# Kernel tuning notes

Measured on AMD Instinct MI355X. Metric: run time of the kernel, lower is better.

## Reference

```python
import jax, jax.numpy as jnp
import numpy as np

N_HEADS = 16
EPS = 1e-6

def setup_inputs() -> dict:
    key = jax.random.key(0)
    k1, k2, k3 = jax.random.split(key, 3)
    B, T, D = 1, 2048, 1024
    x = jax.random.normal(k1, (B, T, D), dtype=jnp.float32)
    # torch nn.Linear weights have shape [out_features, in_features]
    w_qkv = jax.random.normal(k2, (3 * D, D), dtype=jnp.float32) * (1.0 / np.sqrt(D))
    w_out = jax.random.normal(k3, (D, D), dtype=jnp.float32) * (1.0 / np.sqrt(D))
    return {"x": x, "w_qkv": w_qkv, "w_out": w_out}

def reference(x, w_qkv, w_out):
    B, T, D = x.shape
    H = N_HEADS
    Hs = D // H
    qkv = x @ w_qkv.T                              # [B, T, 3D]
    # split_heads with Hs fixed -> 3*H head groups; chunk along head dim gives q,k,v
    qkv = qkv.reshape(B, T, 3, H, Hs).transpose(2, 0, 3, 1, 4)  # [3, B, H, T, Hs]
    q, k, v = qkv[0], qkv[1], qkv[2]
    phi = lambda t: jax.nn.elu(t) + 1.0
    q, k = phi(q), phi(k)
    # causal linear attention (mask=None path): cumulative kv outer products
    k_cumsum = jnp.cumsum(k, axis=2)                           # [B, H, T, Hs]
    kv = jnp.einsum('bhtd,bhtf->bhtdf', k, v)                  # [B, H, T, Hs, Hs]
    kv_cumsum = jnp.cumsum(kv, axis=2)
    q_kv = jnp.einsum('bhtd,bhtdf->bhtf', q, kv_cumsum)        # [B, H, T, Hs]
    q_k_sum = jnp.einsum('bhtd,bhtd->bht', q, k_cumsum)        # [B, H, T]
    xo = q_kv / (q_k_sum[..., None] + EPS)                     # [B, H, T, Hs]
    xo = xo.transpose(0, 2, 1, 3).reshape(B, T, D)             # cat_heads
    return xo @ w_out.T
```

## Files before the change

kernel.cpp:

```cpp
#include <hip/hip_runtime.h>
#include <cmath>

#define T_SEQ 2048
#define HEADS 16
#define HS 64
#define NC 32
#define K2 2048
#define D_MODEL 1024

typedef __attribute__((ext_vector_type(4))) float f32x4;
typedef __attribute__((ext_vector_type(8))) unsigned short u16x8;
typedef __attribute__((ext_vector_type(4))) unsigned short u16x4;

__device__ __forceinline__ unsigned short f2bf_rne(float f){
  unsigned u = __builtin_bit_cast(unsigned, f);
  return (unsigned short)((u + 0x7FFFu + ((u >> 16) & 1u)) >> 16);
}
__device__ __forceinline__ float bf2f(unsigned short h){
  unsigned u = ((unsigned)h) << 16;
  return __builtin_bit_cast(float, u);
}

__global__ __launch_bounds__(256)
void split_all(const float* __restrict__ x, const float* __restrict__ wqkv,
               const float* __restrict__ wout,
               unsigned short* __restrict__ X2, unsigned short* __restrict__ Wq2,
               unsigned short* __restrict__ Wo2)
{
  const int b = blockIdx.x;
  const float* src; unsigned short* dst; int q0;
  if (b < 2048)      { src = x;    dst = X2;  q0 = b; }
  else if (b < 5120) { src = wqkv; dst = Wq2; q0 = b - 2048; }
  else               { src = wout; dst = Wo2; q0 = b - 5120; }
  const int q = q0 * 256 + threadIdx.x;
  float4 v = ((const float4*)src)[q];
  float f[4] = {v.x, v.y, v.z, v.w};
  u16x4 hi, lo;
  #pragma unroll
  for (int i = 0; i < 4; ++i){
    unsigned short h = f2bf_rne(f[i]);
    hi[i] = h;
    lo[i] = f2bf_rne(f[i] - bf2f(h));
  }
  size_t row = (size_t)(q >> 8);
  int c4 = (q & 255) * 4;
  *(u16x4*)(dst + row * K2 + c4) = hi;
  *(u16x4*)(dst + row * K2 + D_MODEL + c4) = lo;
}

__device__ __forceinline__ void gload_lds16(const unsigned short* g, void* l){
  __builtin_amdgcn_global_load_lds((const __attribute__((address_space(1))) unsigned int*)g,
                                   (__attribute__((address_space(3))) unsigned int*)l,
                                   16, 0, 0);
}

__device__ __forceinline__ void mfma_bf16(f32x4& d, u16x8 a, u16x8 b){
  asm("v_mfma_f32_16x16x32_bf16 %0, %1, %2, %0" : "+v"(d) : "v"(a), "v"(b));
}

template<int BM, int EPI>
__global__ __launch_bounds__(256, (BM == 128) ? 2 : 3)
void gemm_split3(const unsigned short* __restrict__ A2,
                 const unsigned short* __restrict__ B2,
                 float* __restrict__ C, int N,
                 float* __restrict__ qkvws)
{
  constexpr int AT = BM * 128;
  constexpr int MI = BM / 32;
  __shared__ unsigned char lds[2 * AT + 32768];

  const int bid = blockIdx.x;
  int bx, by;
  if constexpr (EPI == 1) {
    int swz = (bid & 7) * 48 + (bid >> 3);
    bx = swz >> 4; by = swz & 15;
  } else {
    int swz = (bid & 7) * 32 + (bid >> 3);
    bx = swz >> 5; by = swz & 31;
  }
  const int tileM = by * BM;
  const int tileN = bx * 128;

  const int tid  = threadIdx.x;
  const int lane = tid & 63;
  const int wid  = tid >> 6;
  const int wr   = (wid >> 1) * (BM / 2);
  const int wc   = (wid & 1) * 64;

  f32x4 acc[MI][4];
  #pragma unroll
  for (int i = 0; i < MI; ++i)
    #pragma unroll
    for (int j = 0; j < 4; ++j) acc[i][j] = (f32x4)0.f;

  const int srow = tid >> 3;
  const int kbp  = (tid & 7) << 4;
  const int skb  = kbp ^ ((srow & 7) << 4);
  const unsigned short* Arow = A2 + (size_t)(tileM + srow) * K2 + (skb >> 1);
  const unsigned short* Brow = B2 + (size_t)(tileN + srow) * K2 + (skb >> 1);
  unsigned char* dA = lds + tid * 16;

  #pragma unroll 1
  for (int kt = 0; kt < 16; ++kt){
    const int a_k = kt << 6;
    __syncthreads();
    #pragma unroll
    for (int i = 0; i < MI; ++i){
      gload_lds16(Arow + a_k + (size_t)i * 32 * K2,           dA + i * 4096);
      gload_lds16(Arow + D_MODEL + a_k + (size_t)i * 32 * K2, dA + AT + i * 4096);
    }
    #pragma unroll
    for (int i = 0; i < 4; ++i){
      gload_lds16(Brow + a_k + (size_t)i * 32 * K2,           dA + 2 * AT + i * 4096);
      gload_lds16(Brow + D_MODEL + a_k + (size_t)i * 32 * K2, dA + 2 * AT + 16384 + i * 4096);
    }
    __syncthreads();

    #pragma unroll
    for (int ks = 0; ks < 2; ++ks){
      u16x8 ah[MI], al[MI], bh[4], bl[4];
      #pragma unroll
      for (int mi = 0; mi < MI; ++mi){
        int row = wr + mi * 16 + (lane & 15);
        int kb  = ((ks << 6) + ((lane >> 4) << 4)) ^ ((row & 7) << 4);
        ah[mi] = *(const u16x8*)(lds + row * 128 + kb);
        al[mi] = *(const u16x8*)(lds + AT + row * 128 + kb);
      }
      #pragma unroll
      for (int ni = 0; ni < 4; ++ni){
        int row = wc + ni * 16 + (lane & 15);
        int kb  = ((ks << 6) + ((lane >> 4) << 4)) ^ ((row & 7) << 4);
        bh[ni] = *(const u16x8*)(lds + 2 * AT + row * 128 + kb);
        bl[ni] = *(const u16x8*)(lds + 2 * AT + 16384 + row * 128 + kb);
      }
      #pragma unroll
      for (int mi = 0; mi < MI; ++mi)
        #pragma unroll
        for (int ni = 0; ni < 4; ++ni){
          mfma_bf16(acc[mi][ni], ah[mi], bh[ni]);
          mfma_bf16(acc[mi][ni], ah[mi], bl[ni]);
          mfma_bf16(acc[mi][ni], al[mi], bh[ni]);
        }
    }
  }

  const int r0 = (lane >> 4) << 2;
  const int cl = lane & 15;
  if constexpr (EPI == 0) {
    #pragma unroll
    for (int mi = 0; mi < MI; ++mi){
      int gr = tileM + wr + mi * 16 + r0;
      #pragma unroll
      for (int ni = 0; ni < 4; ++ni){
        int gc = tileN + wc + ni * 16 + cl;
        #pragma unroll
        for (int r = 0; r < 4; ++r) C[(size_t)(gr + r) * N + gc] = acc[mi][ni][r];
      }
    }
  } else {
    #pragma unroll
    for (int ni = 0; ni < 4; ++ni){
      int gc = tileN + wc + ni * 16 + cl;
      int c3 = gc >> 10;
      int hh = (gc >> 6) & 15;
      int s  = gc & 63;
      float* dst = qkvws + ((size_t)(c3 * HEADS + hh) * T_SEQ) * HS + s;
      #pragma unroll
      for (int mi = 0; mi < MI; ++mi){
        int gr = tileM + wr + mi * 16 + r0;
        #pragma unroll
        for (int r = 0; r < 4; ++r){
          float v = acc[mi][ni][r];
          if (c3 < 2) v = (v > 0.f) ? (v + 1.f) : expf(v);
          dst[(size_t)(gr + r) * HS] = v;
        }
      }
    }
  }
}

__global__ __launch_bounds__(256)
void chunk_kv(const float* __restrict__ kbuf, const float* __restrict__ vbuf,
              float* __restrict__ Sc, float* __restrict__ Zc)
{
  const int h = blockIdx.x, c = blockIdx.y;
  const int tid = threadIdx.x;
  const int f = tid & 63, dg = tid >> 6;
  const size_t base = ((size_t)h * T_SEQ + c * 64) * HS;
  float s[16] = {};
  float z = 0.f;
  for (int t = 0; t < 64; ++t) {
    const float vv = vbuf[base + t * HS + f];
    const float* krow = kbuf + base + t * HS + dg * 16;
    float kk4[16];
    #pragma unroll
    for (int r4 = 0; r4 < 4; ++r4)
      *(float4*)&kk4[r4 * 4] = *(const float4*)&krow[r4 * 4];
    #pragma unroll
    for (int r = 0; r < 16; ++r) s[r] += kk4[r] * vv;
    if (dg == 0) z += kbuf[base + t * HS + f];
  }
  float* Sp = Sc + ((size_t)h * NC + c) * (HS * HS);
  #pragma unroll
  for (int r = 0; r < 16; ++r) Sp[(dg * 16 + r) * HS + f] = s[r];
  if (dg == 0) Zc[((size_t)h * NC + c) * HS + f] = z;
}

__global__ __launch_bounds__(256)
void scan_chunks(float* __restrict__ Sc, float* __restrict__ Zc)
{
  const int h = blockIdx.x;
  const int e = blockIdx.y * 256 + threadIdx.x;
  float* p = Sc + ((size_t)h * NC) * (HS * HS) + e;
  float run = 0.f;
  for (int c = 0; c < NC; ++c) {
    float v = p[(size_t)c * HS * HS]; p[(size_t)c * HS * HS] = run; run += v;
  }
  if (blockIdx.y == 0 && threadIdx.x < HS) {
    float* z = Zc + (size_t)h * NC * HS + threadIdx.x;
    float run2 = 0.f;
    for (int c = 0; c < NC; ++c) { float v = z[c * HS]; z[c * HS] = run2; run2 += v; }
  }
}

__global__ __launch_bounds__(256)
void chunk_attn(const float* __restrict__ qbuf, const float* __restrict__ kbuf,
                const float* __restrict__ vbuf, const float* __restrict__ Sc,
                const float* __restrict__ Zc, unsigned short* __restrict__ XO2)
{
  __shared__ float kT[HS][64];
  __shared__ float vl[64][HS + 1];
  __shared__ float Al[64][64];
  const int h = blockIdx.x, c = blockIdx.y;
  const int tid = threadIdx.x;
  const size_t base = ((size_t)h * T_SEQ + c * 64) * HS;

  {
    const int t0 = tid >> 2;
    const int cq = (tid & 3) * 4;
    #pragma unroll
    for (int it = 0; it < 4; ++it) {
      const int col = cq + it * 16;
      float kv[4]; *(float4*)kv = *(const float4*)&kbuf[base + (size_t)t0 * HS + col];
      float vv[4]; *(float4*)vv = *(const float4*)&vbuf[base + (size_t)t0 * HS + col];
      #pragma unroll
      for (int u = 0; u < 4; ++u) { kT[col + u][t0] = kv[u]; vl[t0][col + u] = vv[u]; }
    }
  }
  __syncthreads();

  const int j  = tid & 63;
  const int ig = tid >> 6;

  for (int r = 0; r < 16; ++r) {
    const int i = r * 4 + ig;
    const float* qrow = qbuf + base + (size_t)i * HS;
    float s0 = 0.f, s1 = 0.f, s2 = 0.f, s3 = 0.f;
    #pragma unroll
    for (int d = 0; d < HS; d += 4) {
      float qv[4]; *(float4*)qv = *(const float4*)&qrow[d];
      s0 += qv[0] * kT[d + 0][j];
      s1 += qv[1] * kT[d + 1][j];
      s2 += qv[2] * kT[d + 2][j];
      s3 += qv[3] * kT[d + 3][j];
    }
    Al[i][j] = (j <= i) ? ((s0 + s1) + (s2 + s3)) : 0.f;
  }
  __syncthreads();

  const int f = j;
  const float* Sp = Sc + ((size_t)h * NC + c) * (HS * HS);
  const float* Zp = Zc + ((size_t)h * NC + c) * HS;
  float num[16], den[16];

  for (int r = 0; r < 16; ++r) {
    const int i = r * 4 + ig;
    const float* qrow = qbuf + base + (size_t)i * HS;
    float n0=0.f,n1=0.f,n2=0.f,n3=0.f, e0=0.f,e1=0.f,e2=0.f,e3=0.f;
    #pragma unroll
    for (int d = 0; d < HS; d += 4) {
      float qv[4]; *(float4*)qv = *(const float4*)&qrow[d];
      n0 += qv[0] * Sp[(d + 0) * HS + f];  e0 += qv[0] * Zp[d + 0];
      n1 += qv[1] * Sp[(d + 1) * HS + f];  e1 += qv[1] * Zp[d + 1];
      n2 += qv[2] * Sp[(d + 2) * HS + f];  e2 += qv[2] * Zp[d + 2];
      n3 += qv[3] * Sp[(d + 3) * HS + f];  e3 += qv[3] * Zp[d + 3];
    }
    num[r] = (n0 + n1) + (n2 + n3);
    den[r] = (e0 + e1) + (e2 + e3);
  }

  for (int jj4 = 0; jj4 < 16; ++jj4) {
    float vv[4];
    #pragma unroll
    for (int u = 0; u < 4; ++u) vv[u] = vl[jj4 * 4 + u][f];
    #pragma unroll
    for (int r = 0; r < 16; ++r) {
      const int i = r * 4 + ig;
      float a[4]; *(float4*)a = *(const float4*)&Al[i][jj4 * 4];
      #pragma unroll
      for (int u = 0; u < 4; ++u) { num[r] += a[u] * vv[u]; den[r] += a[u]; }
    }
  }

  #pragma unroll
  for (int r = 0; r < 16; ++r) {
    const int i = r * 4 + ig;
    float val = num[r] / (den[r] + 1e-6f);
    unsigned short hb = f2bf_rne(val);
    unsigned short lb = f2bf_rne(val - bf2f(hb));
    size_t rowoff = (size_t)(c * 64 + i) * K2 + h * 64 + f;
    XO2[rowoff] = hb;
    XO2[rowoff + D_MODEL] = lb;
  }
}

extern "C" void kernel_launch(void* const* d_in, const int* in_sizes, int n_in,
                              void* d_out, int out_size, void* d_ws, size_t ws_size,
                              hipStream_t stream)
{
  (void)in_sizes; (void)n_in; (void)out_size; (void)ws_size;
  const float* x     = (const float*)d_in[0];
  const float* w_qkv = (const float*)d_in[1];
  const float* w_out = (const float*)d_in[2];
  float* out = (float*)d_out;
  char* wsb = (char*)d_ws;

  float* qbuf = (float*)(wsb);
  float* kbuf = (float*)(wsb + ((size_t)8  << 20));
  float* vbuf = (float*)(wsb + ((size_t)16 << 20));
  unsigned short* X2  = (unsigned short*)(wsb + ((size_t)24 << 20));
  float*          Sc  = (float*)(wsb + ((size_t)24 << 20));
  unsigned short* Wq2 = (unsigned short*)(wsb + ((size_t)32 << 20));
  float*          Zc  = (float*)(wsb + ((size_t)32 << 20));
  unsigned short* XO2 = (unsigned short*)(wsb + ((size_t)33 << 20));
  unsigned short* Wo2 = (unsigned short*)(wsb + ((size_t)44 << 20));

  split_all<<<6144, 256, 0, stream>>>(x, w_qkv, w_out, X2, Wq2, Wo2);
  gemm_split3<128, 1><<<384, 256, 0, stream>>>(X2, Wq2, nullptr, 3072, qbuf);
  chunk_kv<<<dim3(16, 32), 256, 0, stream>>>(kbuf, vbuf, Sc, Zc);
  scan_chunks<<<dim3(16, 16), 256, 0, stream>>>(Sc, Zc);
  chunk_attn<<<dim3(16, 32), 256, 0, stream>>>(qbuf, kbuf, vbuf, Sc, Zc, XO2);
  gemm_split3<64, 0><<<256, 256, 0, stream>>>(XO2, Wo2, out, 1024, nullptr);
}
```

Baseline: 217.7 us.

## Move chunked linear-attention stages onto split-bf16 MFMA with transposed layouts

```diff
diff --git a/kernel.cpp b/kernel.cpp
--- a/kernel.cpp
+++ b/kernel.cpp
@@ -25,9 +25,23 @@
 void split_all(const float* __restrict__ x, const float* __restrict__ wqkv,
                const float* __restrict__ wout,
                unsigned short* __restrict__ X2, unsigned short* __restrict__ Wq2,
-               unsigned short* __restrict__ Wo2)
+               unsigned short* __restrict__ Wo2, unsigned short* __restrict__ VT2)
 {
   const int b = blockIdx.x;
+  if (b >= 6144) {
+    int g   = (b - 6144) * 2048 + threadIdx.x * 8;
+    int hh  = g >> 16;
+    int rem = g & 65535;
+    int fi  = rem >> 12;
+    int pl  = (rem >> 11) & 1;
+    int t   = rem & 2047;
+    u16x8 val;
+    unsigned short fill = (fi == 0 && pl == 0) ? (unsigned short)0x3F80 : (unsigned short)0;
+    #pragma unroll
+    for (int e = 0; e < 8; ++e) val[e] = fill;
+    *(u16x8*)(VT2 + ((size_t)((hh * 80 + 64 + fi) * 2 + pl)) * 2048 + t) = val;
+    return;
+  }
   const float* src; unsigned short* dst; int q0;
   if (b < 2048)      { src = x;    dst = X2;  q0 = b; }
   else if (b < 5120) { src = wqkv; dst = Wq2; q0 = b - 2048; }
@@ -63,7 +77,8 @@
 void gemm_split3(const unsigned short* __restrict__ A2,
                  const unsigned short* __restrict__ B2,
                  float* __restrict__ C, int N,
-                 float* __restrict__ qkvws)
+                 unsigned short* __restrict__ Q2, unsigned short* __restrict__ K2k,
+                 unsigned short* __restrict__ kT2, unsigned short* __restrict__ VT2)
 {
   constexpr int AT = BM * 128;
   constexpr int MI = BM / 32;
@@ -164,15 +179,31 @@
       int c3 = gc >> 10;
       int hh = (gc >> 6) & 15;
       int s  = gc & 63;
-      float* dst = qkvws + ((size_t)(c3 * HEADS + hh) * T_SEQ) * HS + s;
       #pragma unroll
       for (int mi = 0; mi < MI; ++mi){
-        int gr = tileM + wr + mi * 16 + r0;
+        int gr0 = tileM + wr + mi * 16 + r0;
+        u16x4 h4, l4;
         #pragma unroll
         for (int r = 0; r < 4; ++r){
           float v = acc[mi][ni][r];
           if (c3 < 2) v = (v > 0.f) ? (v + 1.f) : expf(v);
-          dst[(size_t)(gr + r) * HS] = v;
+          unsigned short hb = f2bf_rne(v);
+          h4[r] = hb;
+          l4[r] = f2bf_rne(v - bf2f(hb));
+        }
+        if (c3 == 0){
+          unsigned short* Qb = Q2 + ((size_t)hh * T_SEQ + gr0) * 128 + s;
+          #pragma unroll
+          for (int r = 0; r < 4; ++r){ Qb[(size_t)r * 128] = h4[r]; Qb[(size_t)r * 128 + 64] = l4[r]; }
+        } else if (c3 == 1){
+          unsigned short* Kb = K2k + ((size_t)hh * T_SEQ + gr0) * 128 + s;
+          #pragma unroll
+          for (int r = 0; r < 4; ++r){ Kb[(size_t)r * 128] = h4[r]; Kb[(size_t)r * 128 + 64] = l4[r]; }
+          *(u16x4*)(kT2 + ((size_t)((hh * 64 + s) * 2 + 0)) * T_SEQ + gr0) = h4;
+          *(u16x4*)(kT2 + ((size_t)((hh * 64 + s) * 2 + 1)) * T_SEQ + gr0) = l4;
+        } else {
+          *(u16x4*)(VT2 + ((size_t)((hh * 80 + s) * 2 + 0)) * T_SEQ + gr0) = h4;
+          *(u16x4*)(VT2 + ((size_t)((hh * 80 + s) * 2 + 1)) * T_SEQ + gr0) = l4;
         }
       }
     }
@@ -180,137 +211,178 @@
 }
 
 __global__ __launch_bounds__(256)
-void chunk_kv(const float* __restrict__ kbuf, const float* __restrict__ vbuf,
-              float* __restrict__ Sc, float* __restrict__ Zc)
-{
-  const int h = blockIdx.x, c = blockIdx.y;
-  const int tid = threadIdx.x;
-  const int f = tid & 63, dg = tid >> 6;
-  const size_t base = ((size_t)h * T_SEQ + c * 64) * HS;
-  float s[16] = {};
-  float z = 0.f;
-  for (int t = 0; t < 64; ++t) {
-    const float vv = vbuf[base + t * HS + f];
-    const float* krow = kbuf + base + t * HS + dg * 16;
-    float kk4[16];
-    #pragma unroll
-    for (int r4 = 0; r4 < 4; ++r4)
-      *(float4*)&kk4[r4 * 4] = *(const float4*)&krow[r4 * 4];
-    #pragma unroll
-    for (int r = 0; r < 16; ++r) s[r] += kk4[r] * vv;
-    if (dg == 0) z += kbuf[base + t * HS + f];
-  }
-  float* Sp = Sc + ((size_t)h * NC + c) * (HS * HS);
-  #pragma unroll
-  for (int r = 0; r < 16; ++r) Sp[(dg * 16 + r) * HS + f] = s[r];
-  if (dg == 0) Zc[((size_t)h * NC + c) * HS + f] = z;
+void chunk_kv_mfma(const unsigned short* __restrict__ VT2,
+                   const unsigned short* __restrict__ kT2,
+                   float* __restrict__ Sc)
+{
+  const int bid = blockIdx.x;
+  const int swz = (bid & 7) * 64 + (bid >> 3);
+  const int h = swz >> 5, c = swz & 31;
+  const int lane = threadIdx.x & 63, w = threadIdx.x >> 6;
+  const int li = lane & 15, hq = lane >> 4;
+  const int bt = c * 64;
+
+  f32x4 acc[5];
+  #pragma unroll
+  for (int mt = 0; mt < 5; ++mt) acc[mt] = (f32x4)0.f;
+
+  const unsigned short* Kb = kT2 + ((size_t)((h * 64 + 16 * w + li) * 2)) * T_SEQ + bt;
+  u16x8 bh[2], bl[2];
+  #pragma unroll
+  for (int ks = 0; ks < 2; ++ks){
+    bh[ks] = *(const u16x8*)(Kb + ks * 32 + hq * 8);
+    bl[ks] = *(const u16x8*)(Kb + T_SEQ + ks * 32 + hq * 8);
+  }
+  #pragma unroll
+  for (int mt = 0; mt < 5; ++mt){
+    const unsigned short* Ab = VT2 + ((size_t)((h * 80 + 16 * mt + li) * 2)) * T_SEQ + bt;
+    #pragma unroll
+    for (int ks = 0; ks < 2; ++ks){
+      u16x8 ah = *(const u16x8*)(Ab + ks * 32 + hq * 8);
+      u16x8 al = *(const u16x8*)(Ab + T_SEQ + ks * 32 + hq * 8);
+      mfma_bf16(acc[mt], ah, bh[ks]);
+      mfma_bf16(acc[mt], ah, bl[ks]);
+      mfma_bf16(acc[mt], al, bh[ks]);
+    }
+  }
+  float* Sp = Sc + ((size_t)(h * 32 + c) * 80) * 64;
+  #pragma unroll
+  for (int mt = 0; mt < 5; ++mt){
+    int f = 16 * mt + 4 * hq;
+    #pragma unroll
+    for (int r = 0; r < 4; ++r)
+      Sp[(size_t)(f + r) * 64 + 16 * w + li] = acc[mt][r];
+  }
 }
 
 __global__ __launch_bounds__(256)
-void scan_chunks(float* __restrict__ Sc, float* __restrict__ Zc)
+void scan_chunks2(const float* __restrict__ Sc, unsigned short* __restrict__ SpT2)
 {
   const int h = blockIdx.x;
   const int e = blockIdx.y * 256 + threadIdx.x;
-  float* p = Sc + ((size_t)h * NC) * (HS * HS) + e;
+  const int f = e >> 6, d = e & 63;
+  unsigned short* Op = SpT2 + ((size_t)(h * 32) * 80 + f) * 128 + d;
+  if (f > 64){
+    for (int c = 0; c < NC; ++c){ Op[0] = 0; Op[64] = 0; Op += (size_t)80 * 128; }
+    return;
+  }
+  const float* Ip = Sc + ((size_t)(h * 32) * 80 + f) * 64 + d;
   float run = 0.f;
-  for (int c = 0; c < NC; ++c) {
-    float v = p[(size_t)c * HS * HS]; p[(size_t)c * HS * HS] = run; run += v;
-  }
-  if (blockIdx.y == 0 && threadIdx.x < HS) {
-    float* z = Zc + (size_t)h * NC * HS + threadIdx.x;
-    float run2 = 0.f;
-    for (int c = 0; c < NC; ++c) { float v = z[c * HS]; z[c * HS] = run2; run2 += v; }
+  for (int c = 0; c < NC; ++c){
+    unsigned short hb = f2bf_rne(run);
+    Op[0]  = hb;
+    Op[64] = f2bf_rne(run - bf2f(hb));
+    run += Ip[0];
+    Ip += (size_t)80 * 64;
+    Op += (size_t)80 * 128;
   }
 }
 
 __global__ __launch_bounds__(256)
-void chunk_attn(const float* __restrict__ qbuf, const float* __restrict__ kbuf,
-                const float* __restrict__ vbuf, const float* __restrict__ Sc,
-                const float* __restrict__ Zc, unsigned short* __restrict__ XO2)
-{
-  __shared__ float kT[HS][64];
-  __shared__ float vl[64][HS + 1];
-  __shared__ float Al[64][64];
-  const int h = blockIdx.x, c = blockIdx.y;
-  const int tid = threadIdx.x;
-  const size_t base = ((size_t)h * T_SEQ + c * 64) * HS;
-
-  {
-    const int t0 = tid >> 2;
-    const int cq = (tid & 3) * 4;
-    #pragma unroll
-    for (int it = 0; it < 4; ++it) {
-      const int col = cq + it * 16;
-      float kv[4]; *(float4*)kv = *(const float4*)&kbuf[base + (size_t)t0 * HS + col];
-      float vv[4]; *(float4*)vv = *(const float4*)&vbuf[base + (size_t)t0 * HS + col];
-      #pragma unroll
-      for (int u = 0; u < 4; ++u) { kT[col + u][t0] = kv[u]; vl[t0][col + u] = vv[u]; }
-    }
-  }
+void chunk_attn_mfma(const unsigned short* __restrict__ Q2,
+                     const unsigned short* __restrict__ K2k,
+                     const unsigned short* __restrict__ VT2,
+                     const unsigned short* __restrict__ SpT2,
+                     unsigned short* __restrict__ XO2)
+{
+  __shared__ unsigned short Pl[64][136];
+  const int bid = blockIdx.x;
+  const int swz = (bid & 7) * 64 + (bid >> 3);
+  const int h = swz >> 5, c = swz & 31;
+  const int lane = threadIdx.x & 63, w = threadIdx.x >> 6;
+  const int li = lane & 15, hq = lane >> 4;
+  const int bt = c * 64;
+
+  const unsigned short* Qp = Q2 + ((size_t)h * T_SEQ + bt + 16 * w + li) * 128;
+  u16x8 qh[2], ql[2];
+  #pragma unroll
+  for (int ks = 0; ks < 2; ++ks){
+    qh[ks] = *(const u16x8*)(Qp + ks * 32 + hq * 8);
+    ql[ks] = *(const u16x8*)(Qp + 64 + ks * 32 + hq * 8);
+  }
+
+  f32x4 accs[4];
+  #pragma unroll
+  for (int nt = 0; nt < 4; ++nt) accs[nt] = (f32x4)0.f;
+  #pragma unroll
+  for (int nt = 0; nt < 4; ++nt){
+    const unsigned short* Kp = K2k + ((size_t)h * T_SEQ + bt + 16 * nt + li) * 128;
+    #pragma unroll
+    for (int ks = 0; ks < 2; ++ks){
+      u16x8 kh = *(const u16x8*)(Kp + ks * 32 + hq * 8);
+      u16x8 kl = *(const u16x8*)(Kp + 64 + ks * 32 + hq * 8);
+      mfma_bf16(accs[nt], qh[ks], kh);
+      mfma_bf16(accs[nt], qh[ks], kl);
+      mfma_bf16(accs[nt], ql[ks], kh);
+    }
+  }
+
+  #pragma unroll
+  for (int nt = 0; nt < 4; ++nt){
+    int i0 = 16 * w + 4 * hq;
+    int j  = 16 * nt + li;
+    #pragma unroll
+    for (int r = 0; r < 4; ++r){
+      float v = (j <= i0 + r) ? accs[nt][r] : 0.f;
+      unsigned short hb = f2bf_rne(v);
+      Pl[i0 + r][j]      = hb;
+      Pl[i0 + r][64 + j] = f2bf_rne(v - bf2f(hb));
+    }
+  }
+
+  f32x4 acco[5];
+  #pragma unroll
+  for (int nt = 0; nt < 5; ++nt) acco[nt] = (f32x4)0.f;
+  const unsigned short* Sb = SpT2 + ((size_t)(h * 32 + c) * 80) * 128;
+  #pragma unroll
+  for (int nt = 0; nt < 5; ++nt){
+    const unsigned short* Sp = Sb + (size_t)(16 * nt + li) * 128;
+    #pragma unroll
+    for (int ks = 0; ks < 2; ++ks){
+      u16x8 sh = *(const u16x8*)(Sp + ks * 32 + hq * 8);
+      u16x8 sl = *(const u16x8*)(Sp + 64 + ks * 32 + hq * 8);
+      mfma_bf16(acco[nt], qh[ks], sh);
+      mfma_bf16(acco[nt], qh[ks], sl);
+      mfma_bf16(acco[nt], ql[ks], sh);
+    }
+  }
+
   __syncthreads();
 
-  const int j  = tid & 63;
-  const int ig = tid >> 6;
-
-  for (int r = 0; r < 16; ++r) {
-    const int i = r * 4 + ig;
-    const float* qrow = qbuf + base + (size_t)i * HS;
-    float s0 = 0.f, s1 = 0.f, s2 = 0.f, s3 = 0.f;
-    #pragma unroll
-    for (int d = 0; d < HS; d += 4) {
-      float qv[4]; *(float4*)qv = *(const float4*)&qrow[d];
-      s0 += qv[0] * kT[d + 0][j];
-      s1 += qv[1] * kT[d + 1][j];
-      s2 += qv[2] * kT[d + 2][j];
-      s3 += qv[3] * kT[d + 3][j];
-    }
-    Al[i][j] = (j <= i) ? ((s0 + s1) + (s2 + s3)) : 0.f;
-  }
-  __syncthreads();
-
-  const int f = j;
-  const float* Sp = Sc + ((size_t)h * NC + c) * (HS * HS);
-  const float* Zp = Zc + ((size_t)h * NC + c) * HS;
-  float num[16], den[16];
-
-  for (int r = 0; r < 16; ++r) {
-    const int i = r * 4 + ig;
-    const float* qrow = qbuf + base + (size_t)i * HS;
-    float n0=0.f,n1=0.f,n2=0.f,n3=0.f, e0=0.f,e1=0.f,e2=0.f,e3=0.f;
-    #pragma unroll
-    for (int d = 0; d < HS; d += 4) {
-      float qv[4]; *(float4*)qv = *(const float4*)&qrow[d];
-      n0 += qv[0] * Sp[(d + 0) * HS + f];  e0 += qv[0] * Zp[d + 0];
-      n1 += qv[1] * Sp[(d + 1) * HS + f];  e1 += qv[1] * Zp[d + 1];
-      n2 += qv[2] * Sp[(d + 2) * HS + f];  e2 += qv[2] * Zp[d + 2];
-      n3 += qv[3] * Sp[(d + 3) * HS + f];  e3 += qv[3] * Zp[d + 3];
-    }
-    num[r] = (n0 + n1) + (n2 + n3);
-    den[r] = (e0 + e1) + (e2 + e3);
-  }
-
-  for (int jj4 = 0; jj4 < 16; ++jj4) {
-    float vv[4];
-    #pragma unroll
-    for (int u = 0; u < 4; ++u) vv[u] = vl[jj4 * 4 + u][f];
-    #pragma unroll
-    for (int r = 0; r < 16; ++r) {
-      const int i = r * 4 + ig;
-      float a[4]; *(float4*)a = *(const float4*)&Al[i][jj4 * 4];
-      #pragma unroll
-      for (int u = 0; u < 4; ++u) { num[r] += a[u] * vv[u]; den[r] += a[u]; }
-    }
-  }
-
-  #pragma unroll
-  for (int r = 0; r < 16; ++r) {
-    const int i = r * 4 + ig;
-    float val = num[r] / (den[r] + 1e-6f);
-    unsigned short hb = f2bf_rne(val);
-    unsigned short lb = f2bf_rne(val - bf2f(hb));
-    size_t rowoff = (size_t)(c * 64 + i) * K2 + h * 64 + f;
-    XO2[rowoff] = hb;
-    XO2[rowoff + D_MODEL] = lb;
+  u16x8 ph[2], plo[2];
+  #pragma unroll
+  for (int ks = 0; ks < 2; ++ks){
+    ph[ks]  = *(const u16x8*)&Pl[16 * w + li][ks * 32 + hq * 8];
+    plo[ks] = *(const u16x8*)&Pl[16 * w + li][64 + ks * 32 + hq * 8];
+  }
+  #pragma unroll
+  for (int nt = 0; nt < 5; ++nt){
+    const unsigned short* Vp = VT2 + ((size_t)((h * 80 + 16 * nt + li) * 2)) * T_SEQ + bt;
+    #pragma unroll
+    for (int ks = 0; ks < 2; ++ks){
+      u16x8 vh = *(const u16x8*)(Vp + ks * 32 + hq * 8);
+      u16x8 vl = *(const u16x8*)(Vp + T_SEQ + ks * 32 + hq * 8);
+      mfma_bf16(acco[nt], ph[ks], vh);
+      mfma_bf16(acco[nt], ph[ks], vl);
+      mfma_bf16(acco[nt], plo[ks], vh);
+    }
+  }
+
+  float dv[4];
+  #pragma unroll
+  for (int r = 0; r < 4; ++r)
+    dv[r] = __shfl(acco[4][r], (lane & 48));
+  #pragma unroll
+  for (int nt = 0; nt < 4; ++nt){
+    int f = 16 * nt + li;
+    #pragma unroll
+    for (int r = 0; r < 4; ++r){
+      int t = bt + 16 * w + 4 * hq + r;
+      float val = acco[nt][r] / (dv[r] + 1e-6f);
+      unsigned short hb = f2bf_rne(val);
+      XO2[(size_t)t * K2 + h * 64 + f]           = hb;
+      XO2[(size_t)t * K2 + D_MODEL + h * 64 + f] = f2bf_rne(val - bf2f(hb));
+    }
   }
 }
 
@@ -324,21 +396,24 @@
   const float* w_out = (const float*)d_in[2];
   float* out = (float*)d_out;
   char* wsb = (char*)d_ws;
-
-  float* qbuf = (float*)(wsb);
-  float* kbuf = (float*)(wsb + ((size_t)8  << 20));
-  float* vbuf = (float*)(wsb + ((size_t)16 << 20));
-  unsigned short* X2  = (unsigned short*)(wsb + ((size_t)24 << 20));
-  float*          Sc  = (float*)(wsb + ((size_t)24 << 20));
-  unsigned short* Wq2 = (unsigned short*)(wsb + ((size_t)32 << 20));
-  float*          Zc  = (float*)(wsb + ((size_t)32 << 20));
-  unsigned short* XO2 = (unsigned short*)(wsb + ((size_t)33 << 20));
-  unsigned short* Wo2 = (unsigned short*)(wsb + ((size_t)44 << 20));
-
-  split_all<<<6144, 256, 0, stream>>>(x, w_qkv, w_out, X2, Wq2, Wo2);
-  gemm_split3<128, 1><<<384, 256, 0, stream>>>(X2, Wq2, nullptr, 3072, qbuf);
-  chunk_kv<<<dim3(16, 32), 256, 0, stream>>>(kbuf, vbuf, Sc, Zc);
-  scan_chunks<<<dim3(16, 16), 256, 0, stream>>>(Sc, Zc);
-  chunk_attn<<<dim3(16, 32), 256, 0, stream>>>(qbuf, kbuf, vbuf, Sc, Zc, XO2);
-  gemm_split3<64, 0><<<256, 256, 0, stream>>>(XO2, Wo2, out, 1024, nullptr);
-}
+  const size_t MiB = (size_t)1 << 20;
+
+  unsigned short* X2   = (unsigned short*)(wsb);
+  unsigned short* Wq2  = (unsigned short*)(wsb + 8  * MiB);
+  float*          Sc   = (float*)(wsb);
+  unsigned short* SpT2 = (unsigned short*)(wsb + 10 * MiB);
+  unsigned short* XO2  = (unsigned short*)(wsb);
+  unsigned short* Q2   = (unsigned short*)(wsb + 21 * MiB);
+  unsigned short* K2k  = (unsigned short*)(wsb + 29 * MiB);
+  unsigned short* kT2  = (unsigned short*)(wsb + 37 * MiB);
+  unsigned short* VT2  = (unsigned short*)(wsb + 45 * MiB);
+  unsigned short* Wo2  = (unsigned short*)(wsb + 55 * MiB);
+
+  split_all<<<6656, 256, 0, stream>>>(x, w_qkv, w_out, X2, Wq2, Wo2, VT2);
+  gemm_split3<128, 1><<<384, 256, 0, stream>>>(X2, Wq2, nullptr, 3072, Q2, K2k, kT2, VT2);
+  chunk_kv_mfma<<<512, 256, 0, stream>>>(VT2, kT2, Sc);
+  scan_chunks2<<<dim3(16, 20), 256, 0, stream>>>(Sc, SpT2);
+  chunk_attn_mfma<<<512, 256, 0, stream>>>(Q2, K2k, VT2, SpT2, XO2);
+  gemm_split3<64, 0><<<256, 256, 0, stream>>>(XO2, Wo2, out, 1024,
+                                              nullptr, nullptr, nullptr, nullptr);
+}
```

After: 183.5 us. 1.19x faster.
